# Kernel tuning notes

Hardware: AMD Instinct MI355X
Metric: run time of the kernel (lower is better)

Reference implementation:

```python
import jax, jax.numpy as jnp
import numpy as np

B, N, F_IN, E_DIM, F, T = 4, 64, 32, 32, 64, 3


def setup_inputs() -> dict:
    key = jax.random.key(0)
    ks = jax.random.split(key, 8)
    X = jax.random.normal(ks[0], (B, N, F_IN), jnp.float32)
    # adjacency mask over the dense N*N ordered-pair layout, broadcast dim 1
    A = (jax.random.uniform(ks[1], (B, N * N, 1)) < 0.25).astype(jnp.float32)
    E = jax.random.normal(ks[2], (B, N * N, E_DIM), jnp.float32)

    def glorot(k, shape):
        fan_in, fan_out = shape
        lim = np.sqrt(6.0 / (fan_in + fan_out)).astype(np.float32)
        return jax.random.uniform(k, shape, jnp.float32, -lim, lim)

    W_embed = glorot(ks[3], (F_IN, F))
    b_embed = jnp.zeros((F,), jnp.float32)
    W_edge = glorot(ks[4], (E_DIM, F * F))
    b_edge = jnp.zeros((F * F,), jnp.float32)
    gru_k = glorot(ks[5], (F, 3 * F))        # input kernel  [F, 3F] (z|r|h)
    gru_rk = glorot(ks[6], (F, 3 * F))       # recurrent kernel
    gru_b = jnp.zeros((3 * F,), jnp.float32)   # input bias
    gru_rb = jnp.zeros((3 * F,), jnp.float32)  # recurrent bias (reset_after)
    return {"X": X, "A": A, "E": E, "W_embed": W_embed, "b_embed": b_embed,
            "W_edge": W_edge, "b_edge": b_edge, "gru_k": gru_k,
            "gru_rk": gru_rk, "gru_b": gru_b, "gru_rb": gru_rb}


def _gru_step(h, x, Wk, Uk, b, rb):
    # Keras GRU cell, reset_after=True: gate order z, r, h
    xg = x @ Wk + b
    hg = h @ Uk + rb
    xz, xr, xh = jnp.split(xg, 3, axis=-1)
    hz, hr, hh = jnp.split(hg, 3, axis=-1)
    z = jax.nn.sigmoid(xz + hz)
    r = jax.nn.sigmoid(xr + hr)
    cand = jnp.tanh(xh + r * hh)
    return z * h + (1.0 - z) * cand


def reference(X, A, E, W_embed, b_embed, W_edge, b_edge,
              gru_k, gru_rk, gru_b, gru_rb):
    H = jax.nn.relu(X @ W_embed + b_embed)            # [B,N,F]
    mask = A.reshape(B, N, N, 1)                      # adjacency mask
    # per-edge transformation matrices (E is constant across T rounds,
    # so the edge MLP is hoisted out of the loop -- same math as original)
    Amat = jax.nn.relu(E @ W_edge + b_edge).reshape(B, N, N, F, F)
    for _ in range(T):
        # message for target i from source j: A_{ij} @ H_j  (batched matvec)
        msgs = jnp.einsum('bnmij,bmj->bnmi', Amat, H)  # [B,N,N,F]
        agg = jnp.sum(msgs * mask, axis=2)             # [B,N,F]
        # GRU over the length-2 sequence [old_state, agg_messages], h0 = 0
        h = jnp.zeros_like(H)
        h = _gru_step(h, H, gru_k, gru_rk, gru_b, gru_rb)
        H = _gru_step(h, agg, gru_k, gru_rk, gru_b, gru_rb)
    return H
```

## Files before the change

### kernel.cpp

```cpp
#include <hip/hip_runtime.h>
#include <math.h>

#define Bv   4
#define Nv   64
#define FIN  32
#define EDIM 32
#define Fv   64
#define NN   (Nv*Nv)

typedef __bf16 bf16x8 __attribute__((ext_vector_type(8)));
typedef float  f32x4  __attribute__((ext_vector_type(4)));

__device__ __forceinline__ float sigmoidf_(float x) {
    return 1.f / (1.f + __expf(-x));
}

__global__ __launch_bounds__(64) void prep_kernel(
    const float* __restrict__ X, const float* __restrict__ W_embed,
    const float* __restrict__ b_embed, const float* __restrict__ A,
    const float* __restrict__ E, const float* __restrict__ W_edge,
    float* __restrict__ H0, __bf16* __restrict__ Wf,
    __bf16* __restrict__ Ebf, int* __restrict__ m_list_g,
    int* __restrict__ cnt_g)
{
    const int blk  = blockIdx.x;
    const int lane = threadIdx.x;

    if (blk < 256) {
        const int nt = blk;
        const int kb = (lane >> 4) * 8;
        const int c  = nt*16 + (lane & 15);
        bf16x8 v;
        #pragma unroll
        for (int t = 0; t < 8; ++t)
            v[t] = (__bf16)W_edge[(kb + t)*4096 + c];
        *(bf16x8*)(Wf + ((size_t)(nt*64 + lane))*8) = v;
    } else if (blk < 512) {
        const int bn = blk - 256;
        const int b  = bn >> 6;
        const int n  = bn & 63;
        __shared__ int ml[Nv];
        __shared__ int cnt_s;
        if (lane == 0) {
            int c = 0;
            const float* arow = A + b*NN + n*Nv;
            for (int m = 0; m < Nv; ++m)
                if (arow[m] != 0.f) ml[c++] = m;
            cnt_s = c;
        }
        __syncthreads();
        const int cnt = cnt_s;
        m_list_g[bn*64 + lane] = (lane < cnt) ? ml[lane] : 0;
        if (lane == 0) cnt_g[bn] = cnt;
        __bf16 row[EDIM];
        if (lane < cnt) {
            const float* er = E + ((size_t)(b*NN + n*Nv + ml[lane]))*EDIM;
            #pragma unroll
            for (int t = 0; t < 8; ++t) {
                const float4 x = *(const float4*)(er + 4*t);
                row[4*t  ] = (__bf16)x.x; row[4*t+1] = (__bf16)x.y;
                row[4*t+2] = (__bf16)x.z; row[4*t+3] = (__bf16)x.w;
            }
        } else {
            #pragma unroll
            for (int e = 0; e < EDIM; ++e) row[e] = (__bf16)0.f;
        }
        __bf16* dst = Ebf + ((size_t)(bn*64 + lane))*EDIM;
        #pragma unroll
        for (int t = 0; t < 4; ++t)
            *(bf16x8*)(dst + 8*t) = *(bf16x8*)(row + 8*t);
    } else {
        const int bn = blk - 512;
        __shared__ float xs[FIN];
        if (lane < FIN) xs[lane] = X[bn*FIN + lane];
        __syncthreads();
        float acc = b_embed[lane];
        #pragma unroll
        for (int k = 0; k < FIN; ++k)
            acc = fmaf(xs[k], W_embed[k*Fv + lane], acc);
        H0[bn*Fv + lane] = fmaxf(acc, 0.f);
    }
}

template<int MTN>
__device__ __forceinline__ void msg_body(
    int bn, int q, int w, int lane,
    const __bf16* __restrict__ Wf, const float* __restrict__ b_edge,
    const __bf16* __restrict__ Ebf, const float (*h_src)[66],
    float* __restrict__ agg_g)
{
    const int c16 = lane & 15;
    const int rg  = (lane >> 4) * 4;
    const int kb  = (lane >> 4) * 8;

    bf16x8 af[MTN];
    #pragma unroll
    for (int mt = 0; mt < MTN; ++mt)
        af[mt] = *(const bf16x8*)(Ebf + ((size_t)(bn*64 + mt*16 + c16))*EDIM + kb);

    float hr[4][MTN][4];
    #pragma unroll
    for (int u = 0; u < 4; ++u)
        #pragma unroll
        for (int mt = 0; mt < MTN; ++mt)
            #pragma unroll
            for (int r = 0; r < 4; ++r)
                hr[u][mt][r] = h_src[mt*16 + rg + r][u*16 + c16];

    #pragma unroll 1
    for (int s = 0; s < 4; ++s) {
        const int i = q*16 + w*4 + s;
        float part = 0.f;
        #pragma unroll
        for (int u = 0; u < 4; ++u) {
            const int nt = i*4 + u;
            const bf16x8 bf = *(const bf16x8*)(Wf + ((size_t)(nt*64 + lane))*8);
            const float  be = b_edge[nt*16 + c16];
            f32x4 cb; cb[0] = be; cb[1] = be; cb[2] = be; cb[3] = be;
            #pragma unroll
            for (int mt = 0; mt < MTN; ++mt) {
                f32x4 d = __builtin_amdgcn_mfma_f32_16x16x32_bf16(af[mt], bf, cb, 0, 0, 0);
                part = fmaf(fmaxf(d[0], 0.f), hr[u][mt][0], part);
                part = fmaf(fmaxf(d[1], 0.f), hr[u][mt][1], part);
                part = fmaf(fmaxf(d[2], 0.f), hr[u][mt][2], part);
                part = fmaf(fmaxf(d[3], 0.f), hr[u][mt][3], part);
            }
        }
        #pragma unroll
        for (int off = 32; off > 0; off >>= 1)
            part += __shfl_xor(part, off);
        if (lane == 0) agg_g[bn*Fv + i] = part;
    }
}

__global__ __launch_bounds__(256, 4) void msg_kernel(
    const float* __restrict__ Hin, const __bf16* __restrict__ Wf,
    const float* __restrict__ b_edge, const __bf16* __restrict__ Ebf,
    const int* __restrict__ m_list_g, const int* __restrict__ cnt_g,
    float* __restrict__ agg_g)
{
    const int bn   = blockIdx.x;
    const int q    = blockIdx.y;
    const int b    = bn >> 6;
    const int tid  = threadIdx.x;
    const int w    = tid >> 6;
    const int lane = tid & 63;

    __shared__ float h_src[Nv][66];

    const int cnt = cnt_g[bn];
    const int Mt  = (cnt + 15) >> 4;
    const int rows = (Mt <= 2) ? 32 : 64;

    const int* ml = m_list_g + bn*64;
    for (int idx = tid; idx < rows*Fv; idx += 256) {
        int a = idx >> 6, j = idx & 63;
        h_src[a][j] = (a < cnt) ? Hin[(b*Nv + ml[a])*Fv + j] : 0.f;
    }
    __syncthreads();

    if (Mt <= 1)      msg_body<1>(bn, q, w, lane, Wf, b_edge, Ebf, h_src, agg_g);
    else if (Mt == 2) msg_body<2>(bn, q, w, lane, Wf, b_edge, Ebf, h_src, agg_g);
    else {
        const int c16 = lane & 15;
        const int rg  = (lane >> 4) * 4;
        const int kb  = (lane >> 4) * 8;
        #pragma unroll 1
        for (int s = 0; s < 4; ++s) {
            const int i = q*16 + w*4 + s;
            float part = 0.f;
            #pragma unroll 1
            for (int u = 0; u < 4; ++u) {
                const int nt = i*4 + u;
                const bf16x8 bf = *(const bf16x8*)(Wf + ((size_t)(nt*64 + lane))*8);
                const float  be = b_edge[nt*16 + c16];
                f32x4 cb; cb[0] = be; cb[1] = be; cb[2] = be; cb[3] = be;
                const int j = u*16 + c16;
                for (int mt = 0; mt < Mt; ++mt) {
                    const bf16x8 a_ = *(const bf16x8*)(Ebf + ((size_t)(bn*64 + mt*16 + c16))*EDIM + kb);
                    f32x4 d = __builtin_amdgcn_mfma_f32_16x16x32_bf16(a_, bf, cb, 0, 0, 0);
                    const int ab = mt*16 + rg;
                    part = fmaf(fmaxf(d[0], 0.f), h_src[ab+0][j], part);
                    part = fmaf(fmaxf(d[1], 0.f), h_src[ab+1][j], part);
                    part = fmaf(fmaxf(d[2], 0.f), h_src[ab+2][j], part);
                    part = fmaf(fmaxf(d[3], 0.f), h_src[ab+3][j], part);
                }
            }
            #pragma unroll
            for (int off = 32; off > 0; off >>= 1)
                part += __shfl_xor(part, off);
            if (lane == 0) agg_g[bn*Fv + i] = part;
        }
    }
}

__global__ __launch_bounds__(192) void gru_kernel(
    const float* __restrict__ Hin, const float* __restrict__ agg_g,
    float* __restrict__ Hout,
    const float* __restrict__ gk, const float* __restrict__ grk,
    const float* __restrict__ gb, const float* __restrict__ grb)
{
    const int bn  = blockIdx.x;
    const int tid = threadIdx.x;

    __shared__ float h_old[Fv];
    __shared__ float aggs[Fv];
    __shared__ float h1[Fv];
    __shared__ float xg[3*Fv];
    __shared__ float hg[3*Fv];

    if (tid < Fv) {
        h_old[tid] = Hin[bn*Fv + tid];
        aggs[tid]  = agg_g[bn*Fv + tid];
    }
    __syncthreads();

    {
        float a0 = 0.f, a1 = 0.f, a2 = 0.f, a3 = 0.f;
        #pragma unroll
        for (int k = 0; k < 16; ++k) {
            a0 = fmaf(h_old[k],      gk[(k     )*192 + tid], a0);
            a1 = fmaf(h_old[k + 16], gk[(k + 16)*192 + tid], a1);
            a2 = fmaf(h_old[k + 32], gk[(k + 32)*192 + tid], a2);
            a3 = fmaf(h_old[k + 48], gk[(k + 48)*192 + tid], a3);
        }
        xg[tid] = gb[tid] + ((a0 + a1) + (a2 + a3));
    }
    __syncthreads();
    if (tid < Fv) {
        float z    = sigmoidf_(xg[tid]       + grb[tid]);
        float r    = sigmoidf_(xg[64 + tid]  + grb[64 + tid]);
        float cand = tanhf    (xg[128 + tid] + r * grb[128 + tid]);
        h1[tid] = (1.f - z) * cand;
    }
    __syncthreads();

    {
        float x0 = 0.f, x1 = 0.f, x2 = 0.f, x3 = 0.f;
        float y0 = 0.f, y1 = 0.f, y2 = 0.f, y3 = 0.f;
        #pragma unroll
        for (int k = 0; k < 16; ++k) {
            x0 = fmaf(aggs[k],      gk [(k     )*192 + tid], x0);
            x1 = fmaf(aggs[k + 16], gk [(k + 16)*192 + tid], x1);
            x2 = fmaf(aggs[k + 32], gk [(k + 32)*192 + tid], x2);
            x3 = fmaf(aggs[k + 48], gk [(k + 48)*192 + tid], x3);
            y0 = fmaf(h1[k],        grk[(k     )*192 + tid], y0);
            y1 = fmaf(h1[k + 16],   grk[(k + 16)*192 + tid], y1);
            y2 = fmaf(h1[k + 32],   grk[(k + 32)*192 + tid], y2);
            y3 = fmaf(h1[k + 48],   grk[(k + 48)*192 + tid], y3);
        }
        xg[tid] = gb[tid]  + ((x0 + x1) + (x2 + x3));
        hg[tid] = grb[tid] + ((y0 + y1) + (y2 + y3));
    }
    __syncthreads();
    if (tid < Fv) {
        float z    = sigmoidf_(xg[tid]       + hg[tid]);
        float r    = sigmoidf_(xg[64 + tid]  + hg[64 + tid]);
        float cand = tanhf    (xg[128 + tid] + r * hg[128 + tid]);
        Hout[bn*Fv + tid] = z * h1[tid] + (1.f - z) * cand;
    }
}

extern "C" void kernel_launch(void* const* d_in, const int* in_sizes, int n_in,
                              void* d_out, int out_size, void* d_ws, size_t ws_size,
                              hipStream_t stream)
{
    const float* X       = (const float*)d_in[0];
    const float* A       = (const float*)d_in[1];
    const float* E       = (const float*)d_in[2];
    const float* W_embed = (const float*)d_in[3];
    const float* b_embed = (const float*)d_in[4];
    const float* W_edge  = (const float*)d_in[5];
    const float* b_edge  = (const float*)d_in[6];
    const float* gk      = (const float*)d_in[7];
    const float* grk     = (const float*)d_in[8];
    const float* gb      = (const float*)d_in[9];
    const float* grb     = (const float*)d_in[10];
    float* out = (float*)d_out;

    float*  H0 = (float*)d_ws;
    float*  H1 = H0 + Bv*Nv*Fv;
    __bf16* Wf = (__bf16*)(H1 + Bv*Nv*Fv);
    __bf16* Ebf = Wf + 256*64*8;
    int*    m_list_g = (int*)(Ebf + (size_t)Bv*Nv*64*EDIM);
    int*    cnt_g = m_list_g + Bv*Nv*64;

    const dim3 mgrid(Bv*Nv, 4);

    prep_kernel<<<768, 64, 0, stream>>>(X, W_embed, b_embed, A, E, W_edge,
                                        H0, Wf, Ebf, m_list_g, cnt_g);

    msg_kernel<<<mgrid, 256, 0, stream>>>(H0, Wf, b_edge, Ebf, m_list_g, cnt_g, out);
    gru_kernel<<<Bv*Nv, 192, 0, stream>>>(H0, out, H1, gk, grk, gb, grb);
    msg_kernel<<<mgrid, 256, 0, stream>>>(H1, Wf, b_edge, Ebf, m_list_g, cnt_g, out);
    gru_kernel<<<Bv*Nv, 192, 0, stream>>>(H1, out, H0, gk, grk, gb, grb);
    msg_kernel<<<mgrid, 256, 0, stream>>>(H0, Wf, b_edge, Ebf, m_list_g, cnt_g, H1);
    gru_kernel<<<Bv*Nv, 192, 0, stream>>>(H0, H1, out, gk, grk, gb, grb);
}
```

Measured before the change: 49.81 us.

## Gather source states directly from global memory and double message grid

```diff
diff --git a/kernel.cpp b/kernel.cpp
--- a/kernel.cpp
+++ b/kernel.cpp
@@ -7,6 +7,7 @@
 #define EDIM 32
 #define Fv   64
 #define NN   (Nv*Nv)
+#define ZROW 256
 
 typedef __bf16 bf16x8 __attribute__((ext_vector_type(8)));
 typedef float  f32x4  __attribute__((ext_vector_type(4)));
@@ -19,9 +20,9 @@
     const float* __restrict__ X, const float* __restrict__ W_embed,
     const float* __restrict__ b_embed, const float* __restrict__ A,
     const float* __restrict__ E, const float* __restrict__ W_edge,
-    float* __restrict__ H0, __bf16* __restrict__ Wf,
-    __bf16* __restrict__ Ebf, int* __restrict__ m_list_g,
-    int* __restrict__ cnt_g)
+    float* __restrict__ H0, float* __restrict__ H1,
+    __bf16* __restrict__ Wf, __bf16* __restrict__ Ebf,
+    int* __restrict__ ml_g, int* __restrict__ cnt_g)
 {
     const int blk  = blockIdx.x;
     const int lane = threadIdx.x;
@@ -35,6 +36,10 @@
         for (int t = 0; t < 8; ++t)
             v[t] = (__bf16)W_edge[(kb + t)*4096 + c];
         *(bf16x8*)(Wf + ((size_t)(nt*64 + lane))*8) = v;
+        if (blk == 0) {
+            H0[ZROW*Fv + lane] = 0.f;
+            H1[ZROW*Fv + lane] = 0.f;
+        }
     } else if (blk < 512) {
         const int bn = blk - 256;
         const int b  = bn >> 6;
@@ -50,7 +55,7 @@
         }
         __syncthreads();
         const int cnt = cnt_s;
-        m_list_g[bn*64 + lane] = (lane < cnt) ? ml[lane] : 0;
+        ml_g[bn*64 + lane] = (lane < cnt) ? (b*Nv + ml[lane]) : ZROW;
         if (lane == 0) cnt_g[bn] = cnt;
         __bf16 row[EDIM];
         if (lane < cnt) {
@@ -84,112 +89,114 @@
 
 template<int MTN>
 __device__ __forceinline__ void msg_body(
-    int bn, int q, int w, int lane,
-    const __bf16* __restrict__ Wf, const float* __restrict__ b_edge,
-    const __bf16* __restrict__ Ebf, const float (*h_src)[66],
-    float* __restrict__ agg_g)
+    int bn, int qq, int w, int lane,
+    const float* __restrict__ Hin, const __bf16* __restrict__ Wf,
+    const float* __restrict__ b_edge, const __bf16* __restrict__ Ebf,
+    const int* __restrict__ ml_g, float* __restrict__ agg_g)
 {
     const int c16 = lane & 15;
     const int rg  = (lane >> 4) * 4;
     const int kb  = (lane >> 4) * 8;
 
     bf16x8 af[MTN];
+    int4   ri[MTN];
     #pragma unroll
-    for (int mt = 0; mt < MTN; ++mt)
+    for (int mt = 0; mt < MTN; ++mt) {
         af[mt] = *(const bf16x8*)(Ebf + ((size_t)(bn*64 + mt*16 + c16))*EDIM + kb);
-
-    float hr[4][MTN][4];
+        ri[mt] = *(const int4*)(ml_g + bn*64 + mt*16 + rg);
+    }
+
+    const int i0 = qq*8 + w*2;
+    float p0 = 0.f, p1 = 0.f;
+
     #pragma unroll
-    for (int u = 0; u < 4; ++u)
-        #pragma unroll
-        for (int mt = 0; mt < MTN; ++mt)
-            #pragma unroll
-            for (int r = 0; r < 4; ++r)
-                hr[u][mt][r] = h_src[mt*16 + rg + r][u*16 + c16];
-
-    #pragma unroll 1
-    for (int s = 0; s < 4; ++s) {
-        const int i = q*16 + w*4 + s;
-        float part = 0.f;
-        #pragma unroll
-        for (int u = 0; u < 4; ++u) {
-            const int nt = i*4 + u;
+    for (int u = 0; u < 4; ++u) {
+        const int jc = u*16 + c16;
+        float hu[MTN][4];
+        #pragma unroll
+        for (int mt = 0; mt < MTN; ++mt) {
+            hu[mt][0] = Hin[ri[mt].x*Fv + jc];
+            hu[mt][1] = Hin[ri[mt].y*Fv + jc];
+            hu[mt][2] = Hin[ri[mt].z*Fv + jc];
+            hu[mt][3] = Hin[ri[mt].w*Fv + jc];
+        }
+        #pragma unroll
+        for (int ii = 0; ii < 2; ++ii) {
+            const int nt = (i0 + ii)*4 + u;
             const bf16x8 bf = *(const bf16x8*)(Wf + ((size_t)(nt*64 + lane))*8);
             const float  be = b_edge[nt*16 + c16];
             f32x4 cb; cb[0] = be; cb[1] = be; cb[2] = be; cb[3] = be;
+            float acc = 0.f;
             #pragma unroll
             for (int mt = 0; mt < MTN; ++mt) {
                 f32x4 d = __builtin_amdgcn_mfma_f32_16x16x32_bf16(af[mt], bf, cb, 0, 0, 0);
-                part = fmaf(fmaxf(d[0], 0.f), hr[u][mt][0], part);
-                part = fmaf(fmaxf(d[1], 0.f), hr[u][mt][1], part);
-                part = fmaf(fmaxf(d[2], 0.f), hr[u][mt][2], part);
-                part = fmaf(fmaxf(d[3], 0.f), hr[u][mt][3], part);
+                acc = fmaf(fmaxf(d[0], 0.f), hu[mt][0], acc);
+                acc = fmaf(fmaxf(d[1], 0.f), hu[mt][1], acc);
+                acc = fmaf(fmaxf(d[2], 0.f), hu[mt][2], acc);
+                acc = fmaf(fmaxf(d[3], 0.f), hu[mt][3], acc);
             }
-        }
-        #pragma unroll
-        for (int off = 32; off > 0; off >>= 1)
-            part += __shfl_xor(part, off);
-        if (lane == 0) agg_g[bn*Fv + i] = part;
-    }
-}
-
-__global__ __launch_bounds__(256, 4) void msg_kernel(
+            if (ii == 0) p0 += acc; else p1 += acc;
+        }
+    }
+    #pragma unroll
+    for (int off = 32; off > 0; off >>= 1) {
+        p0 += __shfl_xor(p0, off);
+        p1 += __shfl_xor(p1, off);
+    }
+    if (lane == 0) {
+        agg_g[bn*Fv + i0]     = p0;
+        agg_g[bn*Fv + i0 + 1] = p1;
+    }
+}
+
+__global__ __launch_bounds__(256) void msg_kernel(
     const float* __restrict__ Hin, const __bf16* __restrict__ Wf,
     const float* __restrict__ b_edge, const __bf16* __restrict__ Ebf,
-    const int* __restrict__ m_list_g, const int* __restrict__ cnt_g,
+    const int* __restrict__ ml_g, const int* __restrict__ cnt_g,
     float* __restrict__ agg_g)
 {
     const int bn   = blockIdx.x;
-    const int q    = blockIdx.y;
-    const int b    = bn >> 6;
+    const int qq   = blockIdx.y;
     const int tid  = threadIdx.x;
     const int w    = tid >> 6;
     const int lane = tid & 63;
 
-    __shared__ float h_src[Nv][66];
-
     const int cnt = cnt_g[bn];
-    const int Mt  = (cnt + 15) >> 4;
-    const int rows = (Mt <= 2) ? 32 : 64;
-
-    const int* ml = m_list_g + bn*64;
-    for (int idx = tid; idx < rows*Fv; idx += 256) {
-        int a = idx >> 6, j = idx & 63;
-        h_src[a][j] = (a < cnt) ? Hin[(b*Nv + ml[a])*Fv + j] : 0.f;
-    }
-    __syncthreads();
-
-    if (Mt <= 1)      msg_body<1>(bn, q, w, lane, Wf, b_edge, Ebf, h_src, agg_g);
-    else if (Mt == 2) msg_body<2>(bn, q, w, lane, Wf, b_edge, Ebf, h_src, agg_g);
-    else {
+    const int Mt  = (cnt == 0) ? 1 : ((cnt + 15) >> 4);
+
+    if (Mt <= 1) {
+        msg_body<1>(bn, qq, w, lane, Hin, Wf, b_edge, Ebf, ml_g, agg_g);
+    } else if (Mt == 2) {
+        msg_body<2>(bn, qq, w, lane, Hin, Wf, b_edge, Ebf, ml_g, agg_g);
+    } else {
         const int c16 = lane & 15;
         const int rg  = (lane >> 4) * 4;
         const int kb  = (lane >> 4) * 8;
-        #pragma unroll 1
-        for (int s = 0; s < 4; ++s) {
-            const int i = q*16 + w*4 + s;
+        const int i0  = qq*8 + w*2;
+        #pragma unroll
+        for (int ii = 0; ii < 2; ++ii) {
             float part = 0.f;
             #pragma unroll 1
             for (int u = 0; u < 4; ++u) {
-                const int nt = i*4 + u;
+                const int jc = u*16 + c16;
+                const int nt = (i0 + ii)*4 + u;
                 const bf16x8 bf = *(const bf16x8*)(Wf + ((size_t)(nt*64 + lane))*8);
                 const float  be = b_edge[nt*16 + c16];
                 f32x4 cb; cb[0] = be; cb[1] = be; cb[2] = be; cb[3] = be;
-                const int j = u*16 + c16;
                 for (int mt = 0; mt < Mt; ++mt) {
                     const bf16x8 a_ = *(const bf16x8*)(Ebf + ((size_t)(bn*64 + mt*16 + c16))*EDIM + kb);
+                    const int4 ri = *(const int4*)(ml_g + bn*64 + mt*16 + rg);
                     f32x4 d = __builtin_amdgcn_mfma_f32_16x16x32_bf16(a_, bf, cb, 0, 0, 0);
-                    const int ab = mt*16 + rg;
-                    part = fmaf(fmaxf(d[0], 0.f), h_src[ab+0][j], part);
-                    part = fmaf(fmaxf(d[1], 0.f), h_src[ab+1][j], part);
-                    part = fmaf(fmaxf(d[2], 0.f), h_src[ab+2][j], part);
-                    part = fmaf(fmaxf(d[3], 0.f), h_src[ab+3][j], part);
+                    part = fmaf(fmaxf(d[0], 0.f), Hin[ri.x*Fv + jc], part);
+                    part = fmaf(fmaxf(d[1], 0.f), Hin[ri.y*Fv + jc], part);
+                    part = fmaf(fmaxf(d[2], 0.f), Hin[ri.z*Fv + jc], part);
+                    part = fmaf(fmaxf(d[3], 0.f), Hin[ri.w*Fv + jc], part);
                 }
             }
             #pragma unroll
             for (int off = 32; off > 0; off >>= 1)
                 part += __shfl_xor(part, off);
-            if (lane == 0) agg_g[bn*Fv + i] = part;
+            if (lane == 0) agg_g[bn*Fv + i0 + ii] = part;
         }
     }
 }
@@ -278,22 +285,22 @@
     const float* grb     = (const float*)d_in[10];
     float* out = (float*)d_out;
 
-    float*  H0 = (float*)d_ws;
-    float*  H1 = H0 + Bv*Nv*Fv;
-    __bf16* Wf = (__bf16*)(H1 + Bv*Nv*Fv);
+    float*  H0  = (float*)d_ws;
+    float*  H1  = H0 + (ZROW + 1)*Fv;
+    __bf16* Wf  = (__bf16*)(H1 + (ZROW + 1)*Fv);
     __bf16* Ebf = Wf + 256*64*8;
-    int*    m_list_g = (int*)(Ebf + (size_t)Bv*Nv*64*EDIM);
-    int*    cnt_g = m_list_g + Bv*Nv*64;
-
-    const dim3 mgrid(Bv*Nv, 4);
+    int*    ml_g  = (int*)(Ebf + (size_t)Bv*Nv*64*EDIM);
+    int*    cnt_g = ml_g + Bv*Nv*64;
+
+    const dim3 mgrid(Bv*Nv, 8);
 
     prep_kernel<<<768, 64, 0, stream>>>(X, W_embed, b_embed, A, E, W_edge,
-                                        H0, Wf, Ebf, m_list_g, cnt_g);
-
-    msg_kernel<<<mgrid, 256, 0, stream>>>(H0, Wf, b_edge, Ebf, m_list_g, cnt_g, out);
+                                        H0, H1, Wf, Ebf, ml_g, cnt_g);
+
+    msg_kernel<<<mgrid, 256, 0, stream>>>(H0, Wf, b_edge, Ebf, ml_g, cnt_g, out);
     gru_kernel<<<Bv*Nv, 192, 0, stream>>>(H0, out, H1, gk, grk, gb, grb);
-    msg_kernel<<<mgrid, 256, 0, stream>>>(H1, Wf, b_edge, Ebf, m_list_g, cnt_g, out);
+    msg_kernel<<<mgrid, 256, 0, stream>>>(H1, Wf, b_edge, Ebf, ml_g, cnt_g, out);
     gru_kernel<<<Bv*Nv, 192, 0, stream>>>(H1, out, H0, gk, grk, gb, grb);
-    msg_kernel<<<mgrid, 256, 0, stream>>>(H0, Wf, b_edge, Ebf, m_list_g, cnt_g, H1);
+    msg_kernel<<<mgrid, 256, 0, stream>>>(H0, Wf, b_edge, Ebf, ml_g, cnt_g, H1);
     gru_kernel<<<Bv*Nv, 192, 0, stream>>>(H0, H1, out, gk, grk, gb, grb);
 }
```

Result: faster. 48.56 us (-2.5%).
